# Kernel tuning notes

Measured on AMD Instinct MI355X. Metric: run time of the kernel, lower is better.

The kernel has to match this reference:

```python
import jax, jax.numpy as jnp
import numpy as np

NUM_HEADS = 8


def setup_inputs() -> dict:
    key = jax.random.key(0)
    k1, k2, k3 = jax.random.split(key, 3)
    B, C, D, H, W = 2, 512, 32, 32, 32
    x = jax.random.normal(k1, (B, C, D, H, W), dtype=jnp.float32)
    w_qkv = jax.random.normal(k2, (3 * C, C), dtype=jnp.float32) * 0.02
    b_qkv = jnp.zeros((3 * C,), dtype=jnp.float32)
    w_out = jax.random.normal(k3, (C, C), dtype=jnp.float32) * 0.02
    b_out = jnp.zeros((C,), dtype=jnp.float32)
    return {"x": x, "w_qkv": w_qkv, "b_qkv": b_qkv, "w_out": w_out, "b_out": b_out}


def reference(x, w_qkv, b_qkv, w_out, b_out):
    B, C, D, H, W = x.shape
    nh = NUM_HEADS
    hd = C // nh
    # 1x1x1 conv3d == pointwise linear over channel dim
    qkv = jnp.einsum('bcdhw,oc->bodhw', x, w_qkv) + b_qkv[None, :, None, None, None]
    q, k, v = jnp.split(qkv, 3, axis=1)  # each [B,C,D,H,W]

    def to_heads(t):
        # [B,C,D,H,W] -> [B,nh,hd,D,H,W] -> [B,H,W,nh,D,hd]
        return t.reshape(B, nh, hd, D, H, W).transpose(0, 4, 5, 1, 3, 2)

    q, k, v = to_heads(q), to_heads(k), to_heads(v)
    scale = hd ** -0.5
    # attention along the depth axis D: attn [B,H,W,nh,D,D]
    attn = jnp.einsum('bhwnic,bhwnjc->bhwnij', q, k) * scale
    attn = jax.nn.softmax(attn, axis=-1)
    out = jnp.einsum('bhwnij,bhwnjc->bhwnic', attn, v)  # [B,H,W,nh,D,hd]
    # [B,H,W,nh,D,hd] -> [B,nh,hd,D,H,W] -> [B,C,D,H,W]
    out = out.transpose(0, 3, 5, 4, 1, 2).reshape(B, C, D, H, W)
    out = jnp.einsum('bcdhw,oc->bodhw', out, w_out) + b_out[None, :, None, None, None]
    return out + x
```

## Files before the change

kernel.cpp:

```cpp
#include <hip/hip_runtime.h>


typedef __bf16 bf16x8 __attribute__((ext_vector_type(8)));
typedef float  f32x4  __attribute__((ext_vector_type(4)));
typedef float  f32x16 __attribute__((ext_vector_type(16)));

__device__ __forceinline__ float b2f(unsigned int u) {
    union { float f; unsigned int i; } x; x.i = u << 16; return x.f;
}
__device__ __forceinline__ unsigned short f2b(float f) {
    union { float f; unsigned int i; } x; x.f = f;
    unsigned int r = x.i + 0x7FFFu + ((x.i >> 16) & 1u);
    return (unsigned short)(r >> 16);
}
__device__ __forceinline__ unsigned int cvtpk(float lo, float hi) {
    unsigned int r;
    asm("v_cvt_pk_bf16_f32 %0, %1, %2" : "=v"(r) : "v"(lo), "v"(hi));
    return r;
}
__device__ __forceinline__ f32x4 mfma16(bf16x8 a, bf16x8 b, f32x4 c) {
    return __builtin_amdgcn_mfma_f32_16x16x32_bf16(a, b, c, 0, 0, 0);
}
__device__ __forceinline__ f32x16 mfma32(bf16x8 a, bf16x8 b, f32x16 c) {
    return __builtin_amdgcn_mfma_f32_32x32x16_bf16(a, b, c, 0, 0, 0);
}
__device__ __forceinline__ void gload16(const void* g, void* l) {
    __builtin_amdgcn_global_load_lds((const unsigned int*)g, (unsigned int*)l, 16, 0, 0);
}

__global__ __launch_bounds__(256) void xprep3(const float* __restrict__ x,
                                              const float* __restrict__ wq_f,
                                              const float* __restrict__ wo_f,
                                              unsigned short* __restrict__ xB,
                                              unsigned short* __restrict__ wT,
                                              unsigned short* __restrict__ wo_bf) {
    const int bid = blockIdx.x;
    const int tid = threadIdx.x;
    if (bid < 2048) {
        __shared__ __align__(16) char tile[32768];
        const int ck = bid & 7, dq = (bid >> 3) & 3, h = (bid >> 5) & 31, b = bid >> 10;

        const int cg = tid & 31;
        const int dl = tid >> 5;
        const int d  = dq * 8 + dl;
        const float* p0 = x + (size_t)b * 16777216 + (size_t)(ck * 64 + cg * 2) * 32768 + d * 1024 + h * 32;
        const float* p1 = p0 + 32768;
        const int cb = (cg * 4) ^ (dl << 4);
        #pragma unroll
        for (int k = 0; k < 8; ++k) {
            float4 a0 = *(const float4*)(p0 + 4 * k);
            float4 a1 = *(const float4*)(p1 + 4 * k);
            *(unsigned int*)(tile + dl * 4096 + (4 * k + 0) * 128 + cb) = cvtpk(a0.x, a1.x);
            *(unsigned int*)(tile + dl * 4096 + (4 * k + 1) * 128 + cb) = cvtpk(a0.y, a1.y);
            *(unsigned int*)(tile + dl * 4096 + (4 * k + 2) * 128 + cb) = cvtpk(a0.z, a1.z);
            *(unsigned int*)(tile + dl * 4096 + (4 * k + 3) * 128 + cb) = cvtpk(a0.w, a1.w);
        }
        __syncthreads();
        const int odl = tid & 7, ot = (tid >> 3) & 7, okb = tid >> 6;
        #pragma unroll
        for (int i = 0; i < 8; ++i) {
            const int wg = i >> 1, kkl = i & 1;
            const int cbyte = (kkl * 64 + okb * 16) ^ (odl << 4);
            uint4 v = *(const uint4*)(tile + odl * 4096 + (wg * 8 + ot) * 128 + cbyte);
            const int G  = (b * 32 + h) * 4 + wg;
            const int kk = ck * 2 + kkl;
            *(uint4*)(xB + (size_t)G * 131072 + kk * 8192 + okb * 2048 +
                      (ot * 32 + dq * 8 + odl) * 8) = v;
        }
    } else {
        const int gidx = (bid - 2048) * 256 + tid;
        if (gidx < 98304) {
            const int r  = gidx % 192;
            const int qd = gidx / 192;
            const int kb = qd & 3, kk = (qd >> 2) & 15, n = qd >> 6;
            const int R  = (r >> 6) * 512 + n * 64 + (r & 63);
            const float* s = wq_f + R * 512 + kk * 32 + kb * 8;
            float4 a0 = *(const float4*)s;
            float4 a1 = *(const float4*)(s + 4);
            *(uint4*)(wT + (size_t)gidx * 8) =
                make_uint4(cvtpk(a0.x, a0.y), cvtpk(a0.z, a0.w), cvtpk(a1.x, a1.y), cvtpk(a1.z, a1.w));
        } else {
            const int g2 = gidx - 98304;
            const float* s = wo_f + (size_t)g2 * 8;
            float4 a0 = *(const float4*)s;
            float4 a1 = *(const float4*)(s + 4);
            *(uint4*)(wo_bf + (size_t)g2 * 8) =
                make_uint4(cvtpk(a0.x, a0.y), cvtpk(a0.z, a0.w), cvtpk(a1.x, a1.y), cvtpk(a1.z, a1.w));
        }
    }
}

__global__ __launch_bounds__(256, 2)
void axial_ab2(const unsigned short* __restrict__ xB,
               const unsigned short* __restrict__ wT,
               const float* __restrict__ bq,
               unsigned short* __restrict__ ao)
{
    __shared__ __align__(16) char lds[58112];
    const int SB0 = 24576, QT0 = 0, KT0 = 16384, VT0 = 32768, P0 = 49152, BIAS0 = 57344;
    float* bias_s = (float*)(lds + BIAS0);

    const int bid = blockIdx.x;
    const int vid = (bid & 7) * 256 + (bid >> 3);
    const int n   = vid & 7;
    const int G   = vid >> 3;
    const int b   = G >> 7, h = (G >> 2) & 31, wg = G & 3;
    const int sbase = b * 32768 + h * 32 + wg * 8;

    const int tid = threadIdx.x;
    const int wv  = tid >> 6;
    const int l   = tid & 63;
    const int l31 = l & 31;
    const int hh  = l >> 5;
    const int wm  = wv >> 1;
    const int wn  = wv & 1;

    const unsigned short* wA = wT + (size_t)n * 98304;
    const unsigned short* xG = xB + (size_t)G * 131072;

    auto stage = [&](int kk, int sl) {
        #pragma unroll
        for (int i = 0; i < 3; ++i) {
            const int j = wv * 3 + i;
            gload16(wA + kk * 6144 + j * 512 + l * 8, lds + sl * 12288 + j * 1024);
        }
        #pragma unroll
        for (int i = 0; i < 4; ++i) {
            const int j = wv * 4 + i;
            gload16(xG + kk * 8192 + j * 512 + l * 8, lds + SB0 + sl * 16384 + j * 1024);
        }
    };

    f32x16 acc[3][4];
    #pragma unroll
    for (int mf = 0; mf < 3; ++mf)
        #pragma unroll
        for (int nf = 0; nf < 4; ++nf) acc[mf][nf] = (f32x16)0.f;

    auto gphase = [&](int sl) {
        #pragma unroll
        for (int ks = 0; ks < 2; ++ks) {
            const int kb = ks * 2 + hh;
            bf16x8 af[3], bfr[4];
            #pragma unroll
            for (int mf = 0; mf < 3; ++mf)
                af[mf] = *(const bf16x8*)(lds + sl * 12288 + kb * 3072 +
                                          (wm * 96 + mf * 32 + l31) * 16);
            #pragma unroll
            for (int nf = 0; nf < 4; ++nf)
                bfr[nf] = *(const bf16x8*)(lds + SB0 + sl * 16384 + kb * 4096 +
                                           (wn * 128 + nf * 32 + l31) * 16);
            #pragma unroll
            for (int mf = 0; mf < 3; ++mf)
                #pragma unroll
                for (int nf = 0; nf < 4; ++nf)
                    acc[mf][nf] = mfma32(af[mf], bfr[nf], acc[mf][nf]);
        }
    };

    stage(0, 0);
    asm volatile("s_waitcnt vmcnt(0)" ::: "memory");
    __builtin_amdgcn_s_barrier();
    __builtin_amdgcn_sched_barrier(0);
    #pragma unroll
    for (int kk = 0; kk < 16; ++kk) {
        if (kk < 15) stage(kk + 1, (kk + 1) & 1);
        __builtin_amdgcn_s_setprio(1);
        gphase(kk & 1);
        __builtin_amdgcn_s_setprio(0);
        asm volatile("s_waitcnt vmcnt(0) lgkmcnt(0)" ::: "memory");
        __builtin_amdgcn_s_barrier();
        __builtin_amdgcn_sched_barrier(0);
    }

    if (tid < 192) bias_s[tid] = bq[(tid >> 6) * 512 + n * 64 + (tid & 63)];
    __syncthreads();

    #pragma unroll
    for (int ph = 0; ph < 2; ++ph) {
        if (wn == ph) {
            #pragma unroll
            for (int mf = 0; mf < 3; ++mf) {
                const int m0 = wm * 96 + mf * 32;
                #pragma unroll
                for (int nf = 0; nf < 4; ++nf) {
                    const int tl = nf;
                    const int d  = l31;
                    const f32x16 v = acc[mf][nf];
                    if (m0 < 128) {
                        const int base = (m0 < 64) ? QT0 : KT0;
                        const int c0g  = (m0 & 63) >> 3;
                        #pragma unroll
                        for (int p = 0; p < 4; ++p) {
                            float4 bb = *(const float4*)(bias_s + m0 + 8 * p + 4 * hh);
                            unsigned int u0 = cvtpk(v[4 * p]     + bb.x, v[4 * p + 1] + bb.y);
                            unsigned int u1 = cvtpk(v[4 * p + 2] + bb.z, v[4 * p + 3] + bb.w);
                            *(uint2*)(lds + base + tl * 4096 + d * 128 +
                                      (((c0g + p) ^ (d & 7)) << 4) + 8 * hh) = make_uint2(u0, u1);
                        }
                    } else {
                        const int e0 = m0 - 128;
                        const int jj = tl * 32 + l31;
                        #pragma unroll
                        for (int reg = 0; reg < 16; ++reg) {
                            const int e = e0 + (reg & 3) + 8 * (reg >> 2) + 4 * hh;
                            *(unsigned short*)(lds + VT0 + e * 256 +
                                               (((jj >> 3) ^ (e & 7)) << 4) + ((2 * jj) & 15)) =
                                f2b(v[reg]);
                        }
                    }
                }
            }
        }
        __syncthreads();

        {
            const int t  = wv;
            const int qg = l >> 4;
            f32x4 sacc[2][2];
            sacc[0][0] = (f32x4)0.f; sacc[0][1] = (f32x4)0.f;
            sacc[1][0] = (f32x4)0.f; sacc[1][1] = (f32x4)0.f;
            #pragma unroll
            for (int kh = 0; kh < 2; ++kh) {
                bf16x8 qa[2], kb_[2];
                #pragma unroll
                for (int mt = 0; mt < 2; ++mt) {
                    const int i = mt * 16 + (l & 15);
                    qa[mt] = *(const bf16x8*)(lds + QT0 + t * 4096 + i * 128 +
                                              (((kh * 4 + qg) ^ (i & 7)) << 4));
                }
                #pragma unroll
                for (int nt = 0; nt < 2; ++nt) {
                    const int jj = nt * 16 + (l & 15);
                    kb_[nt] = *(const bf16x8*)(lds + KT0 + t * 4096 + jj * 128 +
                                               (((kh * 4 + qg) ^ (jj & 7)) << 4));
                }
                #pragma unroll
                for (int mt = 0; mt < 2; ++mt)
                    #pragma unroll
                    for (int nt = 0; nt < 2; ++nt)
                        sacc[mt][nt] = mfma16(qa[mt], kb_[nt], sacc[mt][nt]);
            }
            #pragma unroll
            for (int mt = 0; mt < 2; ++mt) {
                #pragma unroll
                for (int reg = 0; reg < 4; ++reg) {
                    float s0 = sacc[mt][0][reg] * 0.125f;
                    float s1 = sacc[mt][1][reg] * 0.125f;
                    float m = fmaxf(s0, s1);
                    m = fmaxf(m, __shfl_xor(m, 1));
                    m = fmaxf(m, __shfl_xor(m, 2));
                    m = fmaxf(m, __shfl_xor(m, 4));
                    m = fmaxf(m, __shfl_xor(m, 8));
                    float p0 = __expf(s0 - m);
                    float p1 = __expf(s1 - m);
                    float ss = p0 + p1;
                    ss += __shfl_xor(ss, 1);
                    ss += __shfl_xor(ss, 2);
                    ss += __shfl_xor(ss, 4);
                    ss += __shfl_xor(ss, 8);
                    float inv = 1.0f / ss;
                    const int i = mt * 16 + 4 * qg + reg;
                    #pragma unroll
                    for (int nt = 0; nt < 2; ++nt) {
                        const int j = nt * 16 + (l & 15);
                        *(unsigned short*)(lds + P0 + t * 2048 + i * 64 +
                                           (((j >> 3) ^ (i & 3)) << 4) + ((2 * j) & 15)) =
                            f2b((nt ? p1 : p0) * inv);
                    }
                }
            }
            asm volatile("s_waitcnt lgkmcnt(0)" ::: "memory");
            __builtin_amdgcn_sched_barrier(0);

            f32x16 oa[2];
            oa[0] = (f32x16)0.f; oa[1] = (f32x16)0.f;
            #pragma unroll
            for (int ks = 0; ks < 2; ++ks) {
                bf16x8 pb = *(const bf16x8*)(lds + P0 + t * 2048 + l31 * 64 +
                                             (((ks * 2 + hh) ^ (l31 & 3)) << 4));
                #pragma unroll
                for (int cf = 0; cf < 2; ++cf) {
                    const int c = cf * 32 + l31;
                    bf16x8 vv = *(const bf16x8*)(lds + VT0 + c * 256 +
                                                 (((t * 4 + ks * 2 + hh) ^ (c & 7)) << 4));
                    oa[cf] = mfma32(vv, pb, oa[cf]);
                }
            }
            const size_t srow = (size_t)(sbase + l31 * 1024 + ph * 4 + t) * 512 + n * 64;
            #pragma unroll
            for (int cf = 0; cf < 2; ++cf) {
                #pragma unroll
                for (int p = 0; p < 4; ++p) {
                    const int cb = cf * 32 + 8 * p + 4 * hh;
                    float4 bb = *(const float4*)(bias_s + 128 + cb);
                    unsigned int u0 = cvtpk(oa[cf][4 * p]     + bb.x, oa[cf][4 * p + 1] + bb.y);
                    unsigned int u1 = cvtpk(oa[cf][4 * p + 2] + bb.z, oa[cf][4 * p + 3] + bb.w);
                    *(uint2*)(ao + srow + cb) = make_uint2(u0, u1);
                }
            }
        }
        __syncthreads();
    }
}

__global__ __launch_bounds__(256, 2)
void axial_out(const unsigned short* __restrict__ ao,
               const unsigned short* __restrict__ wo,
               const float* __restrict__ bo,
               const float* __restrict__ x,
               float* __restrict__ out)
{
    __shared__ __align__(16) char lds[65536];
    const int bid = blockIdx.x;
    const int vid = (bid & 7) * 256 + (bid >> 3);
    const int mt_ = vid & 3;
    const int nt_ = vid >> 2;
    const int m_base = mt_ * 128;
    const int s_base = nt_ * 128;
    const int bb  = s_base >> 15;
    const int spl = s_base & 32767;
    const float* xblk = x + (size_t)bb * 16777216 + spl;
    float* oblk = out + (size_t)bb * 16777216 + spl;

    const int tid = threadIdx.x;
    const int wv  = tid >> 6;
    const int l   = tid & 63;
    const int l31 = l & 31;
    const int hh  = l >> 5;
    const int wm  = wv >> 1;
    const int wn  = wv & 1;

    auto stage = [&](int kk, int buf) {
        #pragma unroll
        for (int i = 0; i < 4; ++i) {
            const int il  = wv * 4 + i;
            const int row = il * 8 + (l >> 3);
            const unsigned short* srcA = wo + (m_base + row) * 512 + kk * 64 +
                                         (((l & 7) ^ (row & 7)) << 3);
            gload16(srcA, lds + buf * 16384 + il * 1024);
            const unsigned short* srcB = ao + (size_t)(s_base + row) * 512 + kk * 64 +
                                         (((l & 7) ^ (row & 7)) << 3);
            gload16(srcB, lds + 32768 + buf * 16384 + il * 1024);
        }
    };

    f32x16 acc[2][2];
    acc[0][0] = (f32x16)0.f; acc[0][1] = (f32x16)0.f;
    acc[1][0] = (f32x16)0.f; acc[1][1] = (f32x16)0.f;

    stage(0, 0);
    __syncthreads();
    int cur = 0;
    for (int kk = 0; kk < 8; ++kk) {
        if (kk < 7) stage(kk + 1, cur ^ 1);
        #pragma unroll
        for (int ks = 0; ks < 4; ++ks) {
            bf16x8 af[2], bfr[2];
            #pragma unroll
            for (int mf = 0; mf < 2; ++mf) {
                const int row = wm * 64 + mf * 32 + l31;
                af[mf] = *(const bf16x8*)(lds + cur * 16384 + row * 128 +
                                          (((ks * 2 + hh) ^ (row & 7)) << 4));
            }
            #pragma unroll
            for (int nf = 0; nf < 2; ++nf) {
                const int row = wn * 64 + nf * 32 + l31;
                bfr[nf] = *(const bf16x8*)(lds + 32768 + cur * 16384 + row * 128 +
                                           (((ks * 2 + hh) ^ (row & 7)) << 4));
            }
            #pragma unroll
            for (int mf = 0; mf < 2; ++mf)
                #pragma unroll
                for (int nf = 0; nf < 2; ++nf)
                    acc[mf][nf] = mfma32(af[mf], bfr[nf], acc[mf][nf]);
        }
        __syncthreads();
        cur ^= 1;
    }

    #pragma unroll
    for (int mf = 0; mf < 2; ++mf) {
        #pragma unroll
        for (int reg = 0; reg < 16; ++reg) {
            const int co = m_base + wm * 64 + mf * 32 + (reg & 3) + 8 * (reg >> 2) + 4 * hh;
            const float bias = bo[co];
            #pragma unroll
            for (int nf = 0; nf < 2; ++nf) {
                const int sl = wn * 64 + nf * 32 + l31;
                oblk[(size_t)co * 32768 + sl] = acc[mf][nf][reg] + bias +
                                                xblk[(size_t)co * 32768 + sl];
            }
        }
    }
}

__global__ __launch_bounds__(256) void wconvert(const float* __restrict__ wq,
                                                const float* __restrict__ wo,
                                                unsigned short* __restrict__ dst) {
    int i = blockIdx.x * 256 + threadIdx.x;
    const float* src;
    int off;
    if (i < 196608) { src = wq; off = i * 4; }
    else            { src = wo; off = (i - 196608) * 4; }
    float4 v = *(const float4*)(src + off);
    *(uint2*)(dst + (size_t)i * 4) = make_uint2(cvtpk(v.x, v.y), cvtpk(v.z, v.w));
}

__device__ __forceinline__ int adr_qk(int row, int cb) { return row * 2048 + (cb ^ ((row & 7) << 4)); }
__device__ __forceinline__ int adr_x (int row, int cb) { return 98304 + row * 1024 + (cb ^ ((row & 7) << 4)); }
__device__ __forceinline__ int adr_xl(int row, int cb) { return 131072 + row * 1024 + (cb ^ ((row & 7) << 4)); }
__device__ __forceinline__ int adr_v (int e, int jb)   { int a = e * 64 + jb; return 65536 + (a ^ ((e & 7) << 4)); }

__global__ __launch_bounds__(512, 1)
void axial3d_mfma(const float* __restrict__ x,
                  const float* __restrict__ bq,
                  const float* __restrict__ bo,
                  const unsigned short* __restrict__ wq,
                  const unsigned short* __restrict__ wo,
                  float* __restrict__ out) {
    __shared__ char lds[163840];
    const int bid  = blockIdx.x;
    const int work = (bid & 7) * 256 + (bid >> 3);
    const int b    = work >> 10;
    const int h    = (work >> 5) & 31;
    const int w    = work & 31;
    const float* xb = x   + ((size_t)b * 16777216u) + h * 32 + w;
    float*       ob = out + ((size_t)b * 16777216u) + h * 32 + w;
    const int tid  = threadIdx.x;
    const int wv   = tid >> 6;
    const int lane = tid & 63;
    const int g    = lane >> 4;
    const int q    = lane & 15;
    {
        const int d  = tid & 31;
        const int c0 = tid >> 5;
        #pragma unroll
        for (int it = 0; it < 32; ++it) {
            int c = c0 + it * 16;
            float xv = xb[c * 32768 + d * 1024];
            unsigned short hi = f2b(xv);
            unsigned short lo = f2b(xv - b2f(hi));
            *(unsigned short*)(lds + adr_x(d, c * 2))  = hi;
            *(unsigned short*)(lds + adr_xl(d, c * 2)) = lo;
        }
    }
    __syncthreads();
    for (int tp = 0; tp < 3; ++tp) {
        const int mt0 = wv * 12 + tp * 4;
        f32x4 acc[4][2];
        #pragma unroll
        for (int t = 0; t < 4; ++t) { acc[t][0] = (f32x4)0.f; acc[t][1] = (f32x4)0.f; }
        #pragma unroll
        for (int kk = 0; kk < 16; ++kk) {
            bf16x8 bfr[2];
            #pragma unroll
            for (int nt = 0; nt < 2; ++nt)
                bfr[nt] = *(const bf16x8*)(lds + adr_x(nt * 16 + q, kk * 64 + g * 16));
            #pragma unroll
            for (int t = 0; t < 4; ++t) {
                const int o = (mt0 + t) * 16 + q;
                bf16x8 a = *(const bf16x8*)((const char*)wq + o * 1024 + kk * 64 + g * 16);
                acc[t][0] = mfma16(a, bfr[0], acc[t][0]);
                acc[t][1] = mfma16(a, bfr[1], acc[t][1]);
            }
        }
        #pragma unroll
        for (int t = 0; t < 4; ++t) {
            const int mt    = mt0 + t;
            const int obase = mt * 16 + 4 * g;
            float bias[4];
            #pragma unroll
            for (int r = 0; r < 4; ++r) bias[r] = bq[obase + r];
            if (mt < 64) {
                #pragma unroll
                for (int nt = 0; nt < 2; ++nt) {
                    const int d = nt * 16 + q;
                    unsigned int lo = f2b(acc[t][nt][0] + bias[0]) |
                                      ((unsigned int)f2b(acc[t][nt][1] + bias[1]) << 16);
                    unsigned int hi = f2b(acc[t][nt][2] + bias[2]) |
                                      ((unsigned int)f2b(acc[t][nt][3] + bias[3]) << 16);
                    *(uint2*)(lds + adr_qk(d, obase * 2)) = make_uint2(lo, hi);
                }
            } else {
                #pragma unroll
                for (int nt = 0; nt < 2; ++nt) {
                    const int d = nt * 16 + q;
                    #pragma unroll
                    for (int r = 0; r < 4; ++r) {
                        const int e = obase + r - 1024;
                        *(unsigned short*)(lds + adr_v(e, d * 2)) = f2b(acc[t][nt][r] + bias[r]);
                    }
                }
            }
        }
    }
    __syncthreads();
    {
        const int n = wv;
        f32x4 s[2][2];
        s[0][0] = (f32x4)0.f; s[0][1] = (f32x4)0.f;
        s[1][0] = (f32x4)0.f; s[1][1] = (f32x4)0.f;
        #pragma unroll
        for (int kk = 0; kk < 2; ++kk) {
            bf16x8 a0 = *(const bf16x8*)(lds + adr_qk(q,      n * 128 + kk * 64 + g * 16));
            bf16x8 a1 = *(const bf16x8*)(lds + adr_qk(16 + q, n * 128 + kk * 64 + g * 16));
            bf16x8 b0 = *(const bf16x8*)(lds + adr_qk(q,      1024 + n * 128 + kk * 64 + g * 16));
            bf16x8 b1 = *(const bf16x8*)(lds + adr_qk(16 + q, 1024 + n * 128 + kk * 64 + g * 16));
            s[0][0] = mfma16(a0, b0, s[0][0]);
            s[0][1] = mfma16(a0, b1, s[0][1]);
            s[1][0] = mfma16(a1, b0, s[1][0]);
            s[1][1] = mfma16(a1, b1, s[1][1]);
        }
        float pv[2][2][4];
        #pragma unroll
        for (int it = 0; it < 2; ++it) {
            #pragma unroll
            for (int r = 0; r < 4; ++r) {
                float s0 = s[it][0][r] * 0.125f;
                float s1 = s[it][1][r] * 0.125f;
                float m = fmaxf(s0, s1);
                m = fmaxf(m, __shfl_xor(m, 1));
                m = fmaxf(m, __shfl_xor(m, 2));
                m = fmaxf(m, __shfl_xor(m, 4));
                m = fmaxf(m, __shfl_xor(m, 8));
                float p0 = __expf(s0 - m);
                float p1 = __expf(s1 - m);
                float ss = p0 + p1;
                ss += __shfl_xor(ss, 1);
                ss += __shfl_xor(ss, 2);
                ss += __shfl_xor(ss, 4);
                ss += __shfl_xor(ss, 8);
                float inv = 1.0f / ss;
                pv[it][0][r] = p0 * inv;
                pv[it][1][r] = p1 * inv;
            }
        }
        #pragma unroll
        for (int it = 0; it < 2; ++it)
            #pragma unroll
            for (int jt = 0; jt < 2; ++jt)
                #pragma unroll
                for (int r = 0; r < 4; ++r) {
                    const int i = it * 16 + 4 * g + r;
                    *(unsigned short*)(lds + adr_qk(i, n * 128 + (jt * 16 + q) * 2)) =
                        f2b(pv[it][jt][r]);
                }
        asm volatile("s_waitcnt lgkmcnt(0)" ::: "memory");
        __builtin_amdgcn_sched_barrier(0);
        bf16x8 pa0 = *(const bf16x8*)(lds + adr_qk(q,      n * 128 + g * 16));
        bf16x8 pa1 = *(const bf16x8*)(lds + adr_qk(16 + q, n * 128 + g * 16));
        #pragma unroll
        for (int et = 0; et < 4; ++et) {
            const int e = n * 64 + et * 16 + q;
            bf16x8 vb = *(const bf16x8*)(lds + adr_v(e, g * 16));
            f32x4 o0 = mfma16(pa0, vb, (f32x4)0.f);
            f32x4 o1 = mfma16(pa1, vb, (f32x4)0.f);
            const int cb = 1024 + n * 128 + (et * 16 + q) * 2;
            #pragma unroll
            for (int r = 0; r < 4; ++r) {
                *(unsigned short*)(lds + adr_qk(4 * g + r, cb))      = f2b(o0[r]);
                *(unsigned short*)(lds + adr_qk(16 + 4 * g + r, cb)) = f2b(o1[r]);
            }
        }
    }
    __syncthreads();
    for (int p4 = 0; p4 < 4; ++p4) {
        const int mt = wv * 4 + p4;
        f32x4 acc[2];
        acc[0] = (f32x4)0.f; acc[1] = (f32x4)0.f;
        #pragma unroll
        for (int kk = 0; kk < 16; ++kk) {
            bf16x8 b0 = *(const bf16x8*)(lds + adr_qk(q,      1024 + kk * 64 + g * 16));
            bf16x8 b1 = *(const bf16x8*)(lds + adr_qk(16 + q, 1024 + kk * 64 + g * 16));
            bf16x8 a  = *(const bf16x8*)((const char*)wo + (mt * 16 + q) * 1024 + kk * 64 + g * 16);
            acc[0] = mfma16(a, b0, acc[0]);
            acc[1] = mfma16(a, b1, acc[1]);
        }
        const int obase = mt * 16 + 4 * g;
        float bias[4];
        #pragma unroll
        for (int r = 0; r < 4; ++r) bias[r] = bo[obase + r];
        #pragma unroll
        for (int nt = 0; nt < 2; ++nt) {
            const int d = nt * 16 + q;
            uint2 xh = *(const uint2*)(lds + adr_x(d, obase * 2));
            uint2 xl = *(const uint2*)(lds + adr_xl(d, obase * 2));
            float res[4];
            res[0] = b2f(xh.x & 0xffffu) + b2f(xl.x & 0xffffu);
            res[1] = b2f(xh.x >> 16)     + b2f(xl.x >> 16);
            res[2] = b2f(xh.y & 0xffffu) + b2f(xl.y & 0xffffu);
            res[3] = b2f(xh.y >> 16)     + b2f(xl.y >> 16);
            #pragma unroll
            for (int r = 0; r < 4; ++r)
                ob[(obase + r) * 32768 + d * 1024] = acc[nt][r] + bias[r] + res[r];
        }
    }
}

extern "C" void kernel_launch(void* const* d_in, const int* in_sizes, int n_in,
                              void* d_out, int out_size, void* d_ws, size_t ws_size,
                              hipStream_t stream) {
    const float* x     = (const float*)d_in[0];
    const float* w_qkv = (const float*)d_in[1];
    const float* b_qkv = (const float*)d_in[2];
    const float* w_out = (const float*)d_in[3];
    const float* b_out = (const float*)d_in[4];
    float* out = (float*)d_out;

    const size_t XB_OFF = 0;
    const size_t AO_OFF = 67108864;
    const size_t WT_OFF = 134217728;
    const size_t NEED   = 136314880;

    if (ws_size >= NEED) {
        unsigned short* xB    = (unsigned short*)((char*)d_ws + XB_OFF);
        unsigned short* ao    = (unsigned short*)((char*)d_ws + AO_OFF);
        unsigned short* wTt   = (unsigned short*)((char*)d_ws + WT_OFF);
        unsigned short* wo_bf = wTt + 786432;
        xprep3   <<<dim3(2560), dim3(256), 0, stream>>>(x, w_qkv, w_out, xB, wTt, wo_bf);
        axial_ab2<<<dim3(2048), dim3(256), 0, stream>>>(xB, wTt, b_qkv, ao);
        axial_out<<<dim3(2048), dim3(256), 0, stream>>>(ao, wo_bf, b_out, x, out);
    } else {
        unsigned short* wbf = (unsigned short*)d_ws;
        wconvert<<<dim3(1024), dim3(256), 0, stream>>>(w_qkv, w_out, wbf);
        axial3d_mfma<<<dim3(2048), dim3(512), 0, stream>>>(x, b_qkv, b_out,
                                                           wbf, wbf + 786432, out);
    }
}
```

Measured before the change: 273.5 us.

## Halve LDS footprint of QKV-attention kernel via smaller K stages and attention passes

The fused QKV projection plus depth-attention kernel now stages half as much K per step (32 iterations instead of 16), which halves the double-buffered staging area. The attention epilogue runs in four passes of two tokens instead of two passes of four, with each wave handling one token and one half of the channels. Together these cut LDS from about 58KB to about 29KB per block, so more blocks can be resident per CU. In exchange there are twice as many barriers in the GEMM main loop and more epilogue passes with their own synchronisation.

```diff
diff --git a/kernel.cpp b/kernel.cpp
--- a/kernel.cpp
+++ b/kernel.cpp
@@ -91,13 +91,14 @@
 }
 
 __global__ __launch_bounds__(256, 2)
-void axial_ab2(const unsigned short* __restrict__ xB,
+void axial_ab3(const unsigned short* __restrict__ xB,
                const unsigned short* __restrict__ wT,
                const float* __restrict__ bq,
                unsigned short* __restrict__ ao)
 {
-    __shared__ __align__(16) char lds[58112];
-    const int SB0 = 24576, QT0 = 0, KT0 = 16384, VT0 = 32768, P0 = 49152, BIAS0 = 57344;
+    __shared__ __align__(16) char lds[29440];
+    const int SA0 = 0, SB0 = 12288;
+    const int QT0 = 0, KT0 = 8192, VT0 = 16384, P0 = 24576, BIAS0 = 28672;
     float* bias_s = (float*)(lds + BIAS0);
 
     const int bid = blockIdx.x;
@@ -119,15 +120,14 @@
     const unsigned short* xG = xB + (size_t)G * 131072;
 
     auto stage = [&](int kk, int sl) {
-        #pragma unroll
-        for (int i = 0; i < 3; ++i) {
-            const int j = wv * 3 + i;
-            gload16(wA + kk * 6144 + j * 512 + l * 8, lds + sl * 12288 + j * 1024);
-        }
-        #pragma unroll
-        for (int i = 0; i < 4; ++i) {
-            const int j = wv * 4 + i;
-            gload16(xG + kk * 8192 + j * 512 + l * 8, lds + SB0 + sl * 16384 + j * 1024);
+        gload16(wA + kk * 3072 + wv * 512 + l * 8, lds + SA0 + sl * 6144 + wv * 1024);
+        if (wv < 2)
+            gload16(wA + kk * 3072 + (4 + wv) * 512 + l * 8,
+                    lds + SA0 + sl * 6144 + (4 + wv) * 1024);
+        #pragma unroll
+        for (int i = 0; i < 2; ++i) {
+            const int j = wv * 2 + i;
+            gload16(xG + kk * 4096 + j * 512 + l * 8, lds + SB0 + sl * 8192 + j * 1024);
         }
     };
 
@@ -138,24 +138,20 @@
         for (int nf = 0; nf < 4; ++nf) acc[mf][nf] = (f32x16)0.f;
 
     auto gphase = [&](int sl) {
-        #pragma unroll
-        for (int ks = 0; ks < 2; ++ks) {
-            const int kb = ks * 2 + hh;
-            bf16x8 af[3], bfr[4];
-            #pragma unroll
-            for (int mf = 0; mf < 3; ++mf)
-                af[mf] = *(const bf16x8*)(lds + sl * 12288 + kb * 3072 +
-                                          (wm * 96 + mf * 32 + l31) * 16);
+        bf16x8 af[3], bfr[4];
+        #pragma unroll
+        for (int mf = 0; mf < 3; ++mf)
+            af[mf] = *(const bf16x8*)(lds + SA0 + sl * 6144 + hh * 3072 +
+                                      (wm * 96 + mf * 32 + l31) * 16);
+        #pragma unroll
+        for (int nf = 0; nf < 4; ++nf)
+            bfr[nf] = *(const bf16x8*)(lds + SB0 + sl * 8192 + hh * 4096 +
+                                       (wn * 128 + nf * 32 + l31) * 16);
+        #pragma unroll
+        for (int mf = 0; mf < 3; ++mf)
             #pragma unroll
             for (int nf = 0; nf < 4; ++nf)
-                bfr[nf] = *(const bf16x8*)(lds + SB0 + sl * 16384 + kb * 4096 +
-                                           (wn * 128 + nf * 32 + l31) * 16);
-            #pragma unroll
-            for (int mf = 0; mf < 3; ++mf)
-                #pragma unroll
-                for (int nf = 0; nf < 4; ++nf)
-                    acc[mf][nf] = mfma32(af[mf], bfr[nf], acc[mf][nf]);
-        }
+                acc[mf][nf] = mfma32(af[mf], bfr[nf], acc[mf][nf]);
     };
 
     stage(0, 0);
@@ -163,8 +159,8 @@
     __builtin_amdgcn_s_barrier();
     __builtin_amdgcn_sched_barrier(0);
     #pragma unroll
-    for (int kk = 0; kk < 16; ++kk) {
-        if (kk < 15) stage(kk + 1, (kk + 1) & 1);
+    for (int kk = 0; kk < 32; ++kk) {
+        if (kk < 31) stage(kk + 1, (kk + 1) & 1);
         __builtin_amdgcn_s_setprio(1);
         gphase(kk & 1);
         __builtin_amdgcn_s_setprio(0);
@@ -177,26 +173,27 @@
     __syncthreads();
 
     #pragma unroll
-    for (int ph = 0; ph < 2; ++ph) {
-        if (wn == ph) {
+    for (int p = 0; p < 4; ++p) {
+        const int np0 = (p & 1) * 2;
+        if (wn == (p >> 1)) {
             #pragma unroll
             for (int mf = 0; mf < 3; ++mf) {
                 const int m0 = wm * 96 + mf * 32;
                 #pragma unroll
-                for (int nf = 0; nf < 4; ++nf) {
-                    const int tl = nf;
+                for (int tl = 0; tl < 2; ++tl) {
+                    const int nf = np0 + tl;
                     const int d  = l31;
                     const f32x16 v = acc[mf][nf];
                     if (m0 < 128) {
                         const int base = (m0 < 64) ? QT0 : KT0;
                         const int c0g  = (m0 & 63) >> 3;
                         #pragma unroll
-                        for (int p = 0; p < 4; ++p) {
-                            float4 bb = *(const float4*)(bias_s + m0 + 8 * p + 4 * hh);
-                            unsigned int u0 = cvtpk(v[4 * p]     + bb.x, v[4 * p + 1] + bb.y);
-                            unsigned int u1 = cvtpk(v[4 * p + 2] + bb.z, v[4 * p + 3] + bb.w);
+                        for (int q8 = 0; q8 < 4; ++q8) {
+                            float4 bb = *(const float4*)(bias_s + m0 + 8 * q8 + 4 * hh);
+                            unsigned int u0 = cvtpk(v[4 * q8]     + bb.x, v[4 * q8 + 1] + bb.y);
+                            unsigned int u1 = cvtpk(v[4 * q8 + 2] + bb.z, v[4 * q8 + 3] + bb.w);
                             *(uint2*)(lds + base + tl * 4096 + d * 128 +
-                                      (((c0g + p) ^ (d & 7)) << 4) + 8 * hh) = make_uint2(u0, u1);
+                                      (((c0g + q8) ^ (d & 7)) << 4) + 8 * hh) = make_uint2(u0, u1);
                         }
                     } else {
                         const int e0 = m0 - 128;
@@ -204,7 +201,7 @@
                         #pragma unroll
                         for (int reg = 0; reg < 16; ++reg) {
                             const int e = e0 + (reg & 3) + 8 * (reg >> 2) + 4 * hh;
-                            *(unsigned short*)(lds + VT0 + e * 256 +
+                            *(unsigned short*)(lds + VT0 + e * 128 +
                                                (((jj >> 3) ^ (e & 7)) << 4) + ((2 * jj) & 15)) =
                                 f2b(v[reg]);
                         }
@@ -215,7 +212,8 @@
         __syncthreads();
 
         {
-            const int t  = wv;
+            const int tl = wv & 1;
+            const int cf = wv >> 1;
             const int qg = l >> 4;
             f32x4 sacc[2][2];
             sacc[0][0] = (f32x4)0.f; sacc[0][1] = (f32x4)0.f;
@@ -226,13 +224,13 @@
                 #pragma unroll
                 for (int mt = 0; mt < 2; ++mt) {
                     const int i = mt * 16 + (l & 15);
-                    qa[mt] = *(const bf16x8*)(lds + QT0 + t * 4096 + i * 128 +
+                    qa[mt] = *(const bf16x8*)(lds + QT0 + tl * 4096 + i * 128 +
                                               (((kh * 4 + qg) ^ (i & 7)) << 4));
                 }
                 #pragma unroll
                 for (int nt = 0; nt < 2; ++nt) {
                     const int jj = nt * 16 + (l & 15);
-                    kb_[nt] = *(const bf16x8*)(lds + KT0 + t * 4096 + jj * 128 +
+                    kb_[nt] = *(const bf16x8*)(lds + KT0 + tl * 4096 + jj * 128 +
                                                (((kh * 4 + qg) ^ (jj & 7)) << 4));
                 }
                 #pragma unroll
@@ -264,7 +262,7 @@
                     #pragma unroll
                     for (int nt = 0; nt < 2; ++nt) {
                         const int j = nt * 16 + (l & 15);
-                        *(unsigned short*)(lds + P0 + t * 2048 + i * 64 +
+                        *(unsigned short*)(lds + P0 + tl * 2048 + i * 64 +
                                            (((j >> 3) ^ (i & 3)) << 4) + ((2 * j) & 15)) =
                             f2b((nt ? p1 : p0) * inv);
                     }
@@ -273,31 +271,24 @@
             asm volatile("s_waitcnt lgkmcnt(0)" ::: "memory");
             __builtin_amdgcn_sched_barrier(0);
 
-            f32x16 oa[2];
-            oa[0] = (f32x16)0.f; oa[1] = (f32x16)0.f;
+            f32x16 oa = (f32x16)0.f;
             #pragma unroll
             for (int ks = 0; ks < 2; ++ks) {
-                bf16x8 pb = *(const bf16x8*)(lds + P0 + t * 2048 + l31 * 64 +
+                bf16x8 pb = *(const bf16x8*)(lds + P0 + tl * 2048 + l31 * 64 +
                                              (((ks * 2 + hh) ^ (l31 & 3)) << 4));
-                #pragma unroll
-                for (int cf = 0; cf < 2; ++cf) {
-                    const int c = cf * 32 + l31;
-                    bf16x8 vv = *(const bf16x8*)(lds + VT0 + c * 256 +
-                                                 (((t * 4 + ks * 2 + hh) ^ (c & 7)) << 4));
-                    oa[cf] = mfma32(vv, pb, oa[cf]);
-                }
-            }
-            const size_t srow = (size_t)(sbase + l31 * 1024 + ph * 4 + t) * 512 + n * 64;
-            #pragma unroll
-            for (int cf = 0; cf < 2; ++cf) {
-                #pragma unroll
-                for (int p = 0; p < 4; ++p) {
-                    const int cb = cf * 32 + 8 * p + 4 * hh;
-                    float4 bb = *(const float4*)(bias_s + 128 + cb);
-                    unsigned int u0 = cvtpk(oa[cf][4 * p]     + bb.x, oa[cf][4 * p + 1] + bb.y);
-                    unsigned int u1 = cvtpk(oa[cf][4 * p + 2] + bb.z, oa[cf][4 * p + 3] + bb.w);
-                    *(uint2*)(ao + srow + cb) = make_uint2(u0, u1);
-                }
+                const int c = cf * 32 + l31;
+                bf16x8 vv = *(const bf16x8*)(lds + VT0 + c * 128 +
+                                             (((tl * 4 + ks * 2 + hh) ^ (c & 7)) << 4));
+                oa = mfma32(vv, pb, oa);
+            }
+            const size_t srow = (size_t)(sbase + l31 * 1024 + p * 2 + tl) * 512 + n * 64;
+            #pragma unroll
+            for (int q8 = 0; q8 < 4; ++q8) {
+                const int cb = cf * 32 + 8 * q8 + 4 * hh;
+                float4 bb = *(const float4*)(bias_s + 128 + cb);
+                unsigned int u0 = cvtpk(oa[4 * q8]     + bb.x, oa[4 * q8 + 1] + bb.y);
+                unsigned int u1 = cvtpk(oa[4 * q8 + 2] + bb.z, oa[4 * q8 + 3] + bb.w);
+                *(uint2*)(ao + srow + cb) = make_uint2(u0, u1);
             }
         }
         __syncthreads();
@@ -619,7 +610,7 @@
         unsigned short* wTt   = (unsigned short*)((char*)d_ws + WT_OFF);
         unsigned short* wo_bf = wTt + 786432;
         xprep3   <<<dim3(2560), dim3(256), 0, stream>>>(x, w_qkv, w_out, xB, wTt, wo_bf);
-        axial_ab2<<<dim3(2048), dim3(256), 0, stream>>>(xB, wTt, b_qkv, ao);
+        axial_ab3<<<dim3(2048), dim3(256), 0, stream>>>(xB, wTt, b_qkv, ao);
         axial_out<<<dim3(2048), dim3(256), 0, stream>>>(ao, wo_bf, b_out, x, out);
     } else {
         unsigned short* wbf = (unsigned short*)d_ws;
```

After: 295.4 us. 1.08x slower.

## Triple-buffer activation tiles in QKV GEMM to prefetch two stages ahead

Applied to the files above, without the earlier changes.

Splits the staging of weight and activation tiles so that activation (B) tiles use a three-slot LDS ring loaded two k-steps ahead, while weights stay double-buffered. The full vmcnt(0) drain each iteration becomes a partial wait that leaves the newest activation loads in flight, so global latency can overlap with more MFMA work. LDS grows from about 58KB to about 74KB per block, which may reduce how many blocks fit per CU under the 2-blocks launch bound, and the hand-tuned vmcnt counts must match the issue order exactly.

```diff
diff --git a/kernel.cpp b/kernel.cpp
--- a/kernel.cpp
+++ b/kernel.cpp
@@ -91,13 +91,14 @@
 }
 
 __global__ __launch_bounds__(256, 2)
-void axial_ab2(const unsigned short* __restrict__ xB,
+void axial_ab4(const unsigned short* __restrict__ xB,
                const unsigned short* __restrict__ wT,
                const float* __restrict__ bq,
                unsigned short* __restrict__ ao)
 {
-    __shared__ __align__(16) char lds[58112];
-    const int SB0 = 24576, QT0 = 0, KT0 = 16384, VT0 = 32768, P0 = 49152, BIAS0 = 57344;
+    __shared__ __align__(16) char lds[74496];
+    const int SA0 = 0, SB0 = 24576;
+    const int QT0 = 0, KT0 = 16384, VT0 = 32768, P0 = 49152, BIAS0 = 73728;
     float* bias_s = (float*)(lds + BIAS0);
 
     const int bid = blockIdx.x;
@@ -118,12 +119,14 @@
     const unsigned short* wA = wT + (size_t)n * 98304;
     const unsigned short* xG = xB + (size_t)G * 131072;
 
-    auto stage = [&](int kk, int sl) {
+    auto stageA = [&](int kk, int sl) {
         #pragma unroll
         for (int i = 0; i < 3; ++i) {
             const int j = wv * 3 + i;
-            gload16(wA + kk * 6144 + j * 512 + l * 8, lds + sl * 12288 + j * 1024);
-        }
+            gload16(wA + kk * 6144 + j * 512 + l * 8, lds + SA0 + sl * 12288 + j * 1024);
+        }
+    };
+    auto stageB = [&](int kk, int sl) {
         #pragma unroll
         for (int i = 0; i < 4; ++i) {
             const int j = wv * 4 + i;
@@ -137,18 +140,18 @@
         #pragma unroll
         for (int nf = 0; nf < 4; ++nf) acc[mf][nf] = (f32x16)0.f;
 
-    auto gphase = [&](int sl) {
+    auto gphase = [&](int sa, int sb) {
         #pragma unroll
         for (int ks = 0; ks < 2; ++ks) {
             const int kb = ks * 2 + hh;
             bf16x8 af[3], bfr[4];
             #pragma unroll
             for (int mf = 0; mf < 3; ++mf)
-                af[mf] = *(const bf16x8*)(lds + sl * 12288 + kb * 3072 +
+                af[mf] = *(const bf16x8*)(lds + SA0 + sa * 12288 + kb * 3072 +
                                           (wm * 96 + mf * 32 + l31) * 16);
             #pragma unroll
             for (int nf = 0; nf < 4; ++nf)
-                bfr[nf] = *(const bf16x8*)(lds + SB0 + sl * 16384 + kb * 4096 +
+                bfr[nf] = *(const bf16x8*)(lds + SB0 + sb * 16384 + kb * 4096 +
                                            (wn * 128 + nf * 32 + l31) * 16);
             #pragma unroll
             for (int mf = 0; mf < 3; ++mf)
@@ -158,17 +161,21 @@
         }
     };
 
-    stage(0, 0);
-    asm volatile("s_waitcnt vmcnt(0)" ::: "memory");
+    stageA(0, 0); stageB(0, 0); stageB(1, 1);
+    asm volatile("s_waitcnt vmcnt(4)" ::: "memory");
     __builtin_amdgcn_s_barrier();
     __builtin_amdgcn_sched_barrier(0);
+
     #pragma unroll
     for (int kk = 0; kk < 16; ++kk) {
-        if (kk < 15) stage(kk + 1, (kk + 1) & 1);
+        if (kk < 15) stageA(kk + 1, (kk + 1) & 1);
+        if (kk < 14) stageB(kk + 2, (kk + 2) % 3);
         __builtin_amdgcn_s_setprio(1);
-        gphase(kk & 1);
+        gphase(kk & 1, kk % 3);
         __builtin_amdgcn_s_setprio(0);
-        asm volatile("s_waitcnt vmcnt(0) lgkmcnt(0)" ::: "memory");
+        asm volatile("s_waitcnt lgkmcnt(0)" ::: "memory");
+        if (kk < 14)       { asm volatile("s_waitcnt vmcnt(4)" ::: "memory"); }
+        else if (kk == 14) { asm volatile("s_waitcnt vmcnt(0)" ::: "memory"); }
         __builtin_amdgcn_s_barrier();
         __builtin_amdgcn_sched_barrier(0);
     }
@@ -619,7 +626,7 @@
         unsigned short* wTt   = (unsigned short*)((char*)d_ws + WT_OFF);
         unsigned short* wo_bf = wTt + 786432;
         xprep3   <<<dim3(2560), dim3(256), 0, stream>>>(x, w_qkv, w_out, xB, wTt, wo_bf);
-        axial_ab2<<<dim3(2048), dim3(256), 0, stream>>>(xB, wTt, b_qkv, ao);
+        axial_ab4<<<dim3(2048), dim3(256), 0, stream>>>(xB, wTt, b_qkv, ao);
         axial_out<<<dim3(2048), dim3(256), 0, stream>>>(ao, wo_bf, b_out, x, out);
     } else {
         unsigned short* wbf = (unsigned short*)d_ws;
```

Result: no change. 273.2 us, median of 2 (-0.1%).

## Restructure QKV+attention kernel to 512 threads with deeper K-pipelined LDS staging

Applied to the files above, without the earlier changes.

The fused QKV projection and depth-attention kernel moves from 256 to 512 threads with a 2x4 wave grid, so all eight w-columns of attention are handled in a single phase instead of two. The GEMM K-loop now uses 128-wide K tiles with double-buffered A and triple-buffered B. Loads are split across the MMA sub-phases, with partial vmcnt waits and XOR-swizzled LDS rows. The aim is better overlap of global loads with MFMA work and fewer barrier-separated epilogue phases. In exchange LDS use grows to about 148 KB per block, which limits blocks per CU and could reduce occupancy.

```diff
diff --git a/kernel.cpp b/kernel.cpp
--- a/kernel.cpp
+++ b/kernel.cpp
@@ -90,14 +90,15 @@
     }
 }
 
-__global__ __launch_bounds__(256, 2)
-void axial_ab2(const unsigned short* __restrict__ xB,
+__global__ __launch_bounds__(512, 2)
+void axial_ab6(const unsigned short* __restrict__ xB,
                const unsigned short* __restrict__ wT,
                const float* __restrict__ bq,
                unsigned short* __restrict__ ao)
 {
-    __shared__ __align__(16) char lds[58112];
-    const int SB0 = 24576, QT0 = 0, KT0 = 16384, VT0 = 32768, P0 = 49152, BIAS0 = 57344;
+    __shared__ __align__(16) char lds[148224];
+    const int SA0 = 0, SB0 = 49152;
+    const int QT0 = 0, KT0 = 32768, VT0 = 65536, P0 = 98304, BIAS0 = 147456;
     float* bias_s = (float*)(lds + BIAS0);
 
     const int bid = blockIdx.x;
@@ -112,195 +113,207 @@
     const int l   = tid & 63;
     const int l31 = l & 31;
     const int hh  = l >> 5;
-    const int wm  = wv >> 1;
-    const int wn  = wv & 1;
+    const int wm  = wv >> 2;
+    const int wn  = wv & 3;
 
     const unsigned short* wA = wT + (size_t)n * 98304;
     const unsigned short* xG = xB + (size_t)G * 131072;
 
-    auto stage = [&](int kk, int sl) {
-        #pragma unroll
-        for (int i = 0; i < 3; ++i) {
-            const int j = wv * 3 + i;
-            gload16(wA + kk * 6144 + j * 512 + l * 8, lds + sl * 12288 + j * 1024);
-        }
-        #pragma unroll
-        for (int i = 0; i < 4; ++i) {
-            const int j = wv * 4 + i;
-            gload16(xG + kk * 8192 + j * 512 + l * 8, lds + SB0 + sl * 16384 + j * 1024);
-        }
+    if (tid < 192) bias_s[tid] = bq[(tid >> 6) * 512 + n * 64 + (tid & 63)];
+
+    const int gsw = (l & 7) ^ (l >> 3);
+    const int rof = l >> 3;
+
+    auto stageA1 = [&](int t, int buf, int i) {
+        const int j = wv * 3 + i;
+        const int R = j * 8 + rof;
+        const int g = t * 8 + gsw;
+        gload16(wA + (g >> 2) * 6144 + (g & 3) * 1536 + R * 8,
+                lds + SA0 + buf * 24576 + j * 1024 + l * 16);
     };
-
-    f32x16 acc[3][4];
+    auto stageB1 = [&](int t, int buf, int i) {
+        const int j = wv * 4 + i;
+        const int R = j * 8 + rof;
+        const int g = t * 8 + gsw;
+        gload16(xG + (g >> 2) * 8192 + (g & 3) * 2048 + R * 8,
+                lds + SB0 + buf * 32768 + j * 1024 + l * 16);
+    };
+
+    f32x16 acc[3][2];
     #pragma unroll
     for (int mf = 0; mf < 3; ++mf)
         #pragma unroll
-        for (int nf = 0; nf < 4; ++nf) acc[mf][nf] = (f32x16)0.f;
-
-    auto gphase = [&](int sl) {
-        #pragma unroll
-        for (int ks = 0; ks < 2; ++ks) {
-            const int kb = ks * 2 + hh;
-            bf16x8 af[3], bfr[4];
-            #pragma unroll
-            for (int mf = 0; mf < 3; ++mf)
-                af[mf] = *(const bf16x8*)(lds + sl * 12288 + kb * 3072 +
-                                          (wm * 96 + mf * 32 + l31) * 16);
-            #pragma unroll
-            for (int nf = 0; nf < 4; ++nf)
-                bfr[nf] = *(const bf16x8*)(lds + SB0 + sl * 16384 + kb * 4096 +
-                                           (wn * 128 + nf * 32 + l31) * 16);
-            #pragma unroll
-            for (int mf = 0; mf < 3; ++mf)
-                #pragma unroll
-                for (int nf = 0; nf < 4; ++nf)
-                    acc[mf][nf] = mfma32(af[mf], bfr[nf], acc[mf][nf]);
-        }
-    };
-
-    stage(0, 0);
-    asm volatile("s_waitcnt vmcnt(0)" ::: "memory");
+        for (int nf = 0; nf < 2; ++nf) acc[mf][nf] = (f32x16)0.f;
+
+    stageA1(0, 0, 0); stageA1(0, 0, 1); stageA1(0, 0, 2);
+    stageB1(0, 0, 0); stageB1(0, 0, 1); stageB1(0, 0, 2); stageB1(0, 0, 3);
+    stageB1(1, 1, 0); stageB1(1, 1, 1); stageB1(1, 1, 2); stageB1(1, 1, 3);
+    asm volatile("s_waitcnt vmcnt(4)" ::: "memory");
     __builtin_amdgcn_s_barrier();
     __builtin_amdgcn_sched_barrier(0);
+
     #pragma unroll
-    for (int kk = 0; kk < 16; ++kk) {
-        if (kk < 15) stage(kk + 1, (kk + 1) & 1);
-        __builtin_amdgcn_s_setprio(1);
-        gphase(kk & 1);
-        __builtin_amdgcn_s_setprio(0);
-        asm volatile("s_waitcnt vmcnt(0) lgkmcnt(0)" ::: "memory");
-        __builtin_amdgcn_s_barrier();
-        __builtin_amdgcn_sched_barrier(0);
-    }
-
-    if (tid < 192) bias_s[tid] = bq[(tid >> 6) * 512 + n * 64 + (tid & 63)];
-    __syncthreads();
-
-    #pragma unroll
-    for (int ph = 0; ph < 2; ++ph) {
-        if (wn == ph) {
+    for (int t = 0; t < 8; ++t) {
+        const int bufA = t & 1, bufB = t % 3;
+        #pragma unroll
+        for (int ph = 0; ph < 4; ++ph) {
+            bf16x8 af[3], bf[2];
             #pragma unroll
             for (int mf = 0; mf < 3; ++mf) {
-                const int m0 = wm * 96 + mf * 32;
-                #pragma unroll
-                for (int nf = 0; nf < 4; ++nf) {
-                    const int tl = nf;
-                    const int d  = l31;
-                    const f32x16 v = acc[mf][nf];
-                    if (m0 < 128) {
-                        const int base = (m0 < 64) ? QT0 : KT0;
-                        const int c0g  = (m0 & 63) >> 3;
-                        #pragma unroll
-                        for (int p = 0; p < 4; ++p) {
-                            float4 bb = *(const float4*)(bias_s + m0 + 8 * p + 4 * hh);
-                            unsigned int u0 = cvtpk(v[4 * p]     + bb.x, v[4 * p + 1] + bb.y);
-                            unsigned int u1 = cvtpk(v[4 * p + 2] + bb.z, v[4 * p + 3] + bb.w);
-                            *(uint2*)(lds + base + tl * 4096 + d * 128 +
-                                      (((c0g + p) ^ (d & 7)) << 4) + 8 * hh) = make_uint2(u0, u1);
-                        }
-                    } else {
-                        const int e0 = m0 - 128;
-                        const int jj = tl * 32 + l31;
-                        #pragma unroll
-                        for (int reg = 0; reg < 16; ++reg) {
-                            const int e = e0 + (reg & 3) + 8 * (reg >> 2) + 4 * hh;
-                            *(unsigned short*)(lds + VT0 + e * 256 +
-                                               (((jj >> 3) ^ (e & 7)) << 4) + ((2 * jj) & 15)) =
-                                f2b(v[reg]);
-                        }
-                    }
-                }
-            }
-        }
-        __syncthreads();
-
-        {
-            const int t  = wv;
-            const int qg = l >> 4;
-            f32x4 sacc[2][2];
-            sacc[0][0] = (f32x4)0.f; sacc[0][1] = (f32x4)0.f;
-            sacc[1][0] = (f32x4)0.f; sacc[1][1] = (f32x4)0.f;
-            #pragma unroll
-            for (int kh = 0; kh < 2; ++kh) {
-                bf16x8 qa[2], kb_[2];
-                #pragma unroll
-                for (int mt = 0; mt < 2; ++mt) {
-                    const int i = mt * 16 + (l & 15);
-                    qa[mt] = *(const bf16x8*)(lds + QT0 + t * 4096 + i * 128 +
-                                              (((kh * 4 + qg) ^ (i & 7)) << 4));
-                }
-                #pragma unroll
-                for (int nt = 0; nt < 2; ++nt) {
-                    const int jj = nt * 16 + (l & 15);
-                    kb_[nt] = *(const bf16x8*)(lds + KT0 + t * 4096 + jj * 128 +
-                                               (((kh * 4 + qg) ^ (jj & 7)) << 4));
-                }
-                #pragma unroll
-                for (int mt = 0; mt < 2; ++mt)
-                    #pragma unroll
-                    for (int nt = 0; nt < 2; ++nt)
-                        sacc[mt][nt] = mfma16(qa[mt], kb_[nt], sacc[mt][nt]);
-            }
-            #pragma unroll
-            for (int mt = 0; mt < 2; ++mt) {
-                #pragma unroll
-                for (int reg = 0; reg < 4; ++reg) {
-                    float s0 = sacc[mt][0][reg] * 0.125f;
-                    float s1 = sacc[mt][1][reg] * 0.125f;
-                    float m = fmaxf(s0, s1);
-                    m = fmaxf(m, __shfl_xor(m, 1));
-                    m = fmaxf(m, __shfl_xor(m, 2));
-                    m = fmaxf(m, __shfl_xor(m, 4));
-                    m = fmaxf(m, __shfl_xor(m, 8));
-                    float p0 = __expf(s0 - m);
-                    float p1 = __expf(s1 - m);
-                    float ss = p0 + p1;
-                    ss += __shfl_xor(ss, 1);
-                    ss += __shfl_xor(ss, 2);
-                    ss += __shfl_xor(ss, 4);
-                    ss += __shfl_xor(ss, 8);
-                    float inv = 1.0f / ss;
-                    const int i = mt * 16 + 4 * qg + reg;
-                    #pragma unroll
-                    for (int nt = 0; nt < 2; ++nt) {
-                        const int j = nt * 16 + (l & 15);
-                        *(unsigned short*)(lds + P0 + t * 2048 + i * 64 +
-                                           (((j >> 3) ^ (i & 3)) << 4) + ((2 * j) & 15)) =
-                            f2b((nt ? p1 : p0) * inv);
-                    }
-                }
-            }
+                const int r = wm * 96 + mf * 32 + l31;
+                af[mf] = *(const bf16x8*)(lds + SA0 + bufA * 24576 + r * 128 +
+                                          (((ph * 2 + hh) << 4) ^ ((r & 7) << 4)));
+            }
+            #pragma unroll
+            for (int nf = 0; nf < 2; ++nf) {
+                const int r = wn * 64 + nf * 32 + l31;
+                bf[nf] = *(const bf16x8*)(lds + SB0 + bufB * 32768 + r * 128 +
+                                          (((ph * 2 + hh) << 4) ^ ((r & 7) << 4)));
+            }
+            if (ph == 0 && t < 7) { stageA1(t + 1, (t + 1) & 1, 0); stageA1(t + 1, (t + 1) & 1, 1); }
+            if (ph == 1 && t < 7) { stageA1(t + 1, (t + 1) & 1, 2); }
+            if (ph == 1 && t < 6) { stageB1(t + 2, (t + 2) % 3, 0); }
+            if (ph == 2 && t < 6) { stageB1(t + 2, (t + 2) % 3, 1); stageB1(t + 2, (t + 2) % 3, 2); }
+            if (ph == 3 && t < 6) { stageB1(t + 2, (t + 2) % 3, 3); }
+            __builtin_amdgcn_s_barrier();
             asm volatile("s_waitcnt lgkmcnt(0)" ::: "memory");
             __builtin_amdgcn_sched_barrier(0);
-
-            f32x16 oa[2];
-            oa[0] = (f32x16)0.f; oa[1] = (f32x16)0.f;
-            #pragma unroll
-            for (int ks = 0; ks < 2; ++ks) {
-                bf16x8 pb = *(const bf16x8*)(lds + P0 + t * 2048 + l31 * 64 +
-                                             (((ks * 2 + hh) ^ (l31 & 3)) << 4));
-                #pragma unroll
-                for (int cf = 0; cf < 2; ++cf) {
-                    const int c = cf * 32 + l31;
-                    bf16x8 vv = *(const bf16x8*)(lds + VT0 + c * 256 +
-                                                 (((t * 4 + ks * 2 + hh) ^ (c & 7)) << 4));
-                    oa[cf] = mfma32(vv, pb, oa[cf]);
+            __builtin_amdgcn_s_setprio(1);
+            #pragma unroll
+            for (int mf = 0; mf < 3; ++mf)
+                #pragma unroll
+                for (int nf = 0; nf < 2; ++nf)
+                    acc[mf][nf] = mfma32(af[mf], bf[nf], acc[mf][nf]);
+            __builtin_amdgcn_s_setprio(0);
+            if (ph == 3) {
+                if (t < 6)       { asm volatile("s_waitcnt vmcnt(4)" ::: "memory"); }
+                else if (t == 6) { asm volatile("s_waitcnt vmcnt(0)" ::: "memory"); }
+            }
+            __builtin_amdgcn_s_barrier();
+        }
+    }
+    __syncthreads();
+
+    #pragma unroll
+    for (int mf = 0; mf < 3; ++mf) {
+        const int m0 = wm * 96 + mf * 32;
+        #pragma unroll
+        for (int nf = 0; nf < 2; ++nf) {
+            const int tl = wn * 2 + nf;
+            const f32x16 v = acc[mf][nf];
+            if (m0 < 128) {
+                const int base = (m0 < 64) ? QT0 : KT0;
+                const int c0g  = (m0 & 63) >> 3;
+                const int d    = l31;
+                #pragma unroll
+                for (int p = 0; p < 4; ++p) {
+                    float4 bb = *(const float4*)(bias_s + m0 + 8 * p + 4 * hh);
+                    unsigned int u0 = cvtpk(v[4 * p]     + bb.x, v[4 * p + 1] + bb.y);
+                    unsigned int u1 = cvtpk(v[4 * p + 2] + bb.z, v[4 * p + 3] + bb.w);
+                    *(uint2*)(lds + base + tl * 4096 + d * 128 +
+                              (((c0g + p) ^ (d & 7)) << 4) + 8 * hh) = make_uint2(u0, u1);
                 }
-            }
-            const size_t srow = (size_t)(sbase + l31 * 1024 + ph * 4 + t) * 512 + n * 64;
+            } else {
+                const int e0 = m0 - 128;
+                const int jj = tl * 32 + l31;
+                #pragma unroll
+                for (int reg = 0; reg < 16; ++reg) {
+                    const int e = e0 + (reg & 3) + 8 * (reg >> 2) + 4 * hh;
+                    *(unsigned short*)(lds + VT0 + e * 512 +
+                                       (((jj >> 3) ^ (e & 7)) << 4) + ((2 * jj) & 15)) =
+                        f2b(v[reg]);
+                }
+            }
+        }
+    }
+    __syncthreads();
+
+    {
+        const int t   = wv;
+        const int qg  = l >> 4;
+        const int q15 = l & 15;
+        f32x4 sacc[2][2];
+        sacc[0][0] = (f32x4)0.f; sacc[0][1] = (f32x4)0.f;
+        sacc[1][0] = (f32x4)0.f; sacc[1][1] = (f32x4)0.f;
+        #pragma unroll
+        for (int kh = 0; kh < 2; ++kh) {
+            bf16x8 qa[2], kb_[2];
+            #pragma unroll
+            for (int mt = 0; mt < 2; ++mt) {
+                const int i = mt * 16 + q15;
+                qa[mt] = *(const bf16x8*)(lds + QT0 + t * 4096 + i * 128 +
+                                          (((kh * 4 + qg) ^ (i & 7)) << 4));
+            }
+            #pragma unroll
+            for (int nt = 0; nt < 2; ++nt) {
+                const int jj = nt * 16 + q15;
+                kb_[nt] = *(const bf16x8*)(lds + KT0 + t * 4096 + jj * 128 +
+                                           (((kh * 4 + qg) ^ (jj & 7)) << 4));
+            }
+            #pragma unroll
+            for (int mt = 0; mt < 2; ++mt)
+                #pragma unroll
+                for (int nt = 0; nt < 2; ++nt)
+                    sacc[mt][nt] = mfma16(qa[mt], kb_[nt], sacc[mt][nt]);
+        }
+        #pragma unroll
+        for (int mt = 0; mt < 2; ++mt) {
+            #pragma unroll
+            for (int reg = 0; reg < 4; ++reg) {
+                float s0 = sacc[mt][0][reg] * 0.125f;
+                float s1 = sacc[mt][1][reg] * 0.125f;
+                float m = fmaxf(s0, s1);
+                m = fmaxf(m, __shfl_xor(m, 1));
+                m = fmaxf(m, __shfl_xor(m, 2));
+                m = fmaxf(m, __shfl_xor(m, 4));
+                m = fmaxf(m, __shfl_xor(m, 8));
+                float p0 = __expf(s0 - m);
+                float p1 = __expf(s1 - m);
+                float ss = p0 + p1;
+                ss += __shfl_xor(ss, 1);
+                ss += __shfl_xor(ss, 2);
+                ss += __shfl_xor(ss, 4);
+                ss += __shfl_xor(ss, 8);
+                float inv = 1.0f / ss;
+                const int i = mt * 16 + 4 * qg + reg;
+                #pragma unroll
+                for (int nt = 0; nt < 2; ++nt) {
+                    const int j = nt * 16 + q15;
+                    *(unsigned short*)(lds + P0 + t * 2048 + i * 64 +
+                                       (((j >> 3) ^ (i & 3)) << 4) + ((2 * j) & 15)) =
+                        f2b((nt ? p1 : p0) * inv);
+                }
+            }
+        }
+        asm volatile("s_waitcnt lgkmcnt(0)" ::: "memory");
+        __builtin_amdgcn_sched_barrier(0);
+
+        f32x16 oa[2];
+        oa[0] = (f32x16)0.f; oa[1] = (f32x16)0.f;
+        #pragma unroll
+        for (int ks = 0; ks < 2; ++ks) {
+            bf16x8 pb = *(const bf16x8*)(lds + P0 + t * 2048 + l31 * 64 +
+                                         (((ks * 2 + hh) ^ (l31 & 3)) << 4));
             #pragma unroll
             for (int cf = 0; cf < 2; ++cf) {
-                #pragma unroll
-                for (int p = 0; p < 4; ++p) {
-                    const int cb = cf * 32 + 8 * p + 4 * hh;
-                    float4 bb = *(const float4*)(bias_s + 128 + cb);
-                    unsigned int u0 = cvtpk(oa[cf][4 * p]     + bb.x, oa[cf][4 * p + 1] + bb.y);
-                    unsigned int u1 = cvtpk(oa[cf][4 * p + 2] + bb.z, oa[cf][4 * p + 3] + bb.w);
-                    *(uint2*)(ao + srow + cb) = make_uint2(u0, u1);
-                }
-            }
-        }
-        __syncthreads();
+                const int c = cf * 32 + l31;
+                bf16x8 vv = *(const bf16x8*)(lds + VT0 + c * 512 +
+                                             (((t * 4 + ks * 2 + hh) ^ (c & 7)) << 4));
+                oa[cf] = mfma32(vv, pb, oa[cf]);
+            }
+        }
+        const size_t srow = (size_t)(sbase + l31 * 1024 + t) * 512 + n * 64;
+        #pragma unroll
+        for (int cf = 0; cf < 2; ++cf) {
+            #pragma unroll
+            for (int p = 0; p < 4; ++p) {
+                const int cb = cf * 32 + 8 * p + 4 * hh;
+                float4 bb = *(const float4*)(bias_s + 128 + cb);
+                unsigned int u0 = cvtpk(oa[cf][4 * p]     + bb.x, oa[cf][4 * p + 1] + bb.y);
+                unsigned int u1 = cvtpk(oa[cf][4 * p + 2] + bb.z, oa[cf][4 * p + 3] + bb.w);
+                *(uint2*)(ao + srow + cb) = make_uint2(u0, u1);
+            }
+        }
     }
 }
 
@@ -619,7 +632,7 @@
         unsigned short* wTt   = (unsigned short*)((char*)d_ws + WT_OFF);
         unsigned short* wo_bf = wTt + 786432;
         xprep3   <<<dim3(2560), dim3(256), 0, stream>>>(x, w_qkv, w_out, xB, wTt, wo_bf);
-        axial_ab2<<<dim3(2048), dim3(256), 0, stream>>>(xB, wTt, b_qkv, ao);
+        axial_ab6<<<dim3(2048), dim3(512), 0, stream>>>(xB, wTt, b_qkv, ao);
         axial_out<<<dim3(2048), dim3(256), 0, stream>>>(ao, wo_bf, b_out, x, out);
     } else {
         unsigned short* wbf = (unsigned short*)d_ws;
```

New measurement: 303.6 us. 1.11x slower.
